# Kernel optimization log

Measured on AMD Instinct MI355X. Metric: run time of the kernel, lower is better.

## Reference

```python
import jax, jax.numpy as jnp
import numpy as np

# Model constants (from init_kwargs, post tensor-parallel split with world_size=8)
N_LOCAL_HEADS = 4      # 32 // 8
N_LOCAL_KV_HEADS = 1   # 8 // 8
N_REP = 4              # local q heads per kv head
HEAD_DIM = 128         # 4096 // 32
ROPE_THETA = 500000.0
EPS = 1e-6
FLOOR_SCALE = 8192.0
ATTN_SCALE = 0.1


def setup_inputs() -> dict:
    key = jax.random.key(0)
    ks = jax.random.split(key, 5)
    B, S, D = 4, 2048, 4096
    x = jax.random.normal(ks[0], (B, S, D), dtype=jnp.float32)
    positions = jnp.arange(S, dtype=jnp.int32)
    w_std = 0.02
    wq = jax.random.normal(ks[1], (D, N_LOCAL_HEADS * HEAD_DIM), dtype=jnp.float32) * w_std
    wk = jax.random.normal(ks[2], (D, N_LOCAL_KV_HEADS * HEAD_DIM), dtype=jnp.float32) * w_std
    wv = jax.random.normal(ks[3], (D, N_LOCAL_KV_HEADS * HEAD_DIM), dtype=jnp.float32) * w_std
    wo = jax.random.normal(ks[4], (N_LOCAL_HEADS * HEAD_DIM, D), dtype=jnp.float32) * w_std
    return {"x": x, "positions": positions, "wq": wq, "wk": wk, "wv": wv, "wo": wo}


def _apply_rope(t, cos, sin):
    # t: [B, S, h, HEAD_DIM]; interleaved complex pairs as in torch view_as_complex
    B, S, h, hd = t.shape
    tr = t.reshape(B, S, h, hd // 2, 2)
    t0, t1 = tr[..., 0], tr[..., 1]
    c = cos[None, :, None, :]  # [1, S, 1, hd//2]
    s = sin[None, :, None, :]
    o0 = t0 * c - t1 * s
    o1 = t0 * s + t1 * c
    return jnp.stack([o0, o1], axis=-1).reshape(B, S, h, hd)


def _rms_norm(t):
    # QK-norm: L2/RMS norm over head_dim, no learnable weight (Llama4 style)
    return t * jax.lax.rsqrt(jnp.mean(t * t, axis=-1, keepdims=True) + EPS)


def reference(x, positions, wq, wk, wv, wo):
    B, S, D = x.shape
    q = (x @ wq).reshape(B, S, N_LOCAL_HEADS, HEAD_DIM)
    k = (x @ wk).reshape(B, S, N_LOCAL_KV_HEADS, HEAD_DIM)
    v = (x @ wv).reshape(B, S, N_LOCAL_KV_HEADS, HEAD_DIM)

    # RoPE angles
    pos_f = positions.astype(jnp.float32)
    inv_freq = 1.0 / (ROPE_THETA ** (jnp.arange(0, HEAD_DIM, 2, dtype=jnp.float32) / HEAD_DIM))
    ang = pos_f[:, None] * inv_freq[None, :]  # [S, HEAD_DIM//2]
    cos, sin = jnp.cos(ang), jnp.sin(ang)

    q = _apply_rope(q, cos, sin)
    k = _apply_rope(k, cos, sin)

    # QK RMSNorm (applied after rope)
    q = _rms_norm(q)
    k = _rms_norm(k)

    # Temperature-tuned query scaling (per absolute position)
    attn_scales = jnp.log(jnp.floor((pos_f + 1.0) / FLOOR_SCALE) + 1.0) * ATTN_SCALE + 1.0
    q = q * attn_scales[None, :, None, None]

    # GQA: repeat kv heads to match local query heads
    k = jnp.repeat(k, N_REP, axis=2)  # [B, S, H, hd]
    v = jnp.repeat(v, N_REP, axis=2)

    scale = 1.0 / jnp.sqrt(jnp.float32(HEAD_DIM))
    scores = jnp.einsum("bqhd,bkhd->bhqk", q, k) * scale  # [B, H, S, S]
    causal = jnp.tril(jnp.ones((S, S), dtype=bool))
    scores = jnp.where(causal[None, None, :, :], scores, jnp.finfo(scores.dtype).min)
    probs = jax.nn.softmax(scores, axis=-1)
    attn = jnp.einsum("bhqk,bkhd->bqhd", probs, v).reshape(B, S, N_LOCAL_HEADS * HEAD_DIM)
    return attn @ wo
```

## Files before the change

kernel.cpp:

```cpp
#include <hip/hip_runtime.h>

typedef unsigned short u16;
typedef unsigned int u32;
typedef __bf16 bf16x8 __attribute__((ext_vector_type(8)));
typedef float f32x4 __attribute__((ext_vector_type(4)));

#define S_LEN 2048

__device__ __forceinline__ u16 f2b(float f) {
    union { float f; unsigned u; } a; a.f = f;
    unsigned u = a.u;
    unsigned r = u + 0x7fffu + ((u >> 16) & 1u);
    return (u16)(r >> 16);
}

__device__ __forceinline__ u32 pk2(float a, float b) {
    return (u32)f2b(a) | ((u32)f2b(b) << 16);
}

__device__ __forceinline__ void gload16(const void* g, void* l) {
    __builtin_amdgcn_global_load_lds(
        (const __attribute__((address_space(1))) unsigned int*)g,
        (__attribute__((address_space(3))) unsigned int*)l,
        16, 0, 0);
}

__global__ __launch_bounds__(256) void conv_x_kernel(const float* __restrict__ x,
                                                     u16* __restrict__ xb) {
    long i = ((long)blockIdx.x * 256 + threadIdx.x) * 4;
    float4 v = *(const float4*)(x + i);
    ushort4 o;
    o.x = f2b(v.x); o.y = f2b(v.y); o.z = f2b(v.z); o.w = f2b(v.w);
    *(ushort4*)(xb + i) = o;
}

__global__ __launch_bounds__(256) void pack_wqkv_kernel(const float* __restrict__ wq,
                                                        const float* __restrict__ wk,
                                                        const float* __restrict__ wv,
                                                        u16* __restrict__ W) {
    __shared__ float t[32][33];
    const int n0 = blockIdx.x * 32, k0 = blockIdx.y * 32;
    const int tid = threadIdx.x;
    const int cc = tid & 31, rr = tid >> 5;
    #pragma unroll
    for (int i = 0; i < 4; ++i) {
        int k = k0 + rr + i * 8, n = n0 + cc;
        float v;
        if (n < 512)      v = wq[(size_t)k * 512 + n];
        else if (n < 640) v = wk[(size_t)k * 128 + (n - 512)];
        else              v = wv[(size_t)k * 128 + (n - 640)];
        t[rr + i * 8][cc] = v;
    }
    __syncthreads();
    #pragma unroll
    for (int i = 0; i < 4; ++i) {
        int nn = rr + i * 8, kk = cc;
        W[(size_t)(n0 + nn) * 4096 + k0 + kk] = f2b(t[kk][nn]);
    }
}

__global__ __launch_bounds__(256) void pack_wo_kernel(const float* __restrict__ wo,
                                                      u16* __restrict__ W) {
    __shared__ float t[32][33];
    const int n0 = blockIdx.x * 32, k0 = blockIdx.y * 32;
    const int tid = threadIdx.x;
    const int cc = tid & 31, rr = tid >> 5;
    #pragma unroll
    for (int i = 0; i < 4; ++i)
        t[rr + i * 8][cc] = wo[(size_t)(k0 + rr + i * 8) * 4096 + n0 + cc];
    __syncthreads();
    #pragma unroll
    for (int i = 0; i < 4; ++i)
        W[(size_t)(n0 + rr + i * 8) * 512 + k0 + cc] = f2b(t[cc][rr + i * 8]);
}

__global__ __launch_bounds__(256) void gemm_bf16(const u16* __restrict__ A,
                                                 const u16* __restrict__ B,
                                                 float* __restrict__ C0,
                                                 float* __restrict__ C1,
                                                 int M, int N, int K, int kLen) {
    __shared__ __align__(16) u16 sA[128 * 32];
    __shared__ __align__(16) u16 sB[128 * 32];
    const int tid = threadIdx.x;
    const int lane = tid & 63, wid = tid >> 6;
    const int wr = wid >> 1, wc = wid & 1;
    const int l15 = lane & 15, g = lane >> 4;
    const int srow = (lane >> 2), scol = (lane & 3) * 8;

    const u32 lid = blockIdx.x + gridDim.x * (blockIdx.y + gridDim.y * blockIdx.z);
    const u32 xcd = lid & 7, slot = lid >> 3;
    const u32 per = gridDim.x * gridDim.z;
    const u32 bml = slot / per;
    const u32 r   = slot - bml * per;
    const int bn  = r % gridDim.x;
    const int z   = r / gridDim.x;
    const int bm  = xcd * (gridDim.y >> 3) + bml;

    float* C = z ? C1 : C0;
    const int k0 = z * kLen;

    f32x4 acc[4][4] = {};

    for (int kt = k0; kt < k0 + kLen; kt += 32) {
        __syncthreads();
        #pragma unroll
        for (int i = 0; i < 2; ++i) {
            int ch = wid * 2 + i;
            int rw = ch * 16 + srow;
            gload16(&A[(size_t)(bm * 128 + rw) * K + kt + scol], &sA[ch * 512]);
            gload16(&B[(size_t)(bn * 128 + rw) * K + kt + scol], &sB[ch * 512]);
        }
        __syncthreads();
        bf16x8 af[4], bfr[4];
        #pragma unroll
        for (int m = 0; m < 4; ++m)
            af[m] = *(const bf16x8*)&sA[(wr * 64 + m * 16 + l15) * 32 + g * 8];
        #pragma unroll
        for (int n = 0; n < 4; ++n)
            bfr[n] = *(const bf16x8*)&sB[(wc * 64 + n * 16 + l15) * 32 + g * 8];
        #pragma unroll
        for (int m = 0; m < 4; ++m)
            #pragma unroll
            for (int n = 0; n < 4; ++n)
                acc[m][n] = __builtin_amdgcn_mfma_f32_16x16x32_bf16(af[m], bfr[n], acc[m][n], 0, 0, 0);
    }

    #pragma unroll
    for (int m = 0; m < 4; ++m) {
        int row = bm * 128 + wr * 64 + m * 16 + g * 4;
        #pragma unroll
        for (int n = 0; n < 4; ++n) {
            int col = bn * 128 + wc * 64 + n * 16 + l15;
            #pragma unroll
            for (int rr = 0; rr < 4; ++rr)
                C[(size_t)(row + rr) * N + col] = acc[m][n][rr];
        }
    }
}

__global__ __launch_bounds__(256) void rope_rms_kernel(const float* __restrict__ P0,
                                                       const float* __restrict__ P1,
                                                       const int* __restrict__ positions,
                                                       u16* __restrict__ Qb,
                                                       u16* __restrict__ Kb) {
    const int w = blockIdx.x * 4 + (threadIdx.x >> 6);
    const int lane = threadIdx.x & 63;
    const int row = w / 5, head = w - row * 5;
    const int s = row & (S_LEN - 1);

    float pos = (float)positions[s];
    float ex = (float)(2 * lane) * (1.0f / 128.0f);
    float inv_freq = __expf(-ex * 13.122363377404328f);
    float ang = pos * inv_freq;
    float c, sn;
    __sincosf(ang, &sn, &c);

    size_t off = (size_t)row * 768 + head * 128 + 2 * lane;
    float2 va = *(const float2*)&P0[off];
    float2 vb = *(const float2*)&P1[off];
    float x0 = va.x + vb.x, x1 = va.y + vb.y;
    float o0 = x0 * c - x1 * sn;
    float o1 = x0 * sn + x1 * c;

    float ss = o0 * o0 + o1 * o1;
    #pragma unroll
    for (int m = 1; m < 64; m <<= 1) ss += __shfl_xor(ss, m, 64);
    float rms = rsqrtf(ss * (1.0f / 128.0f) + 1e-6f);

    if (head < 4) {
        float ascale = logf(floorf((pos + 1.0f) * (1.0f / 8192.0f)) + 1.0f) * 0.1f + 1.0f;
        float mult = rms * ascale * 0.12751743f;
        *(u32*)&Qb[(size_t)row * 512 + head * 128 + 2 * lane] = pk2(o0 * mult, o1 * mult);
    } else {
        *(u32*)&Kb[(size_t)row * 128 + 2 * lane] = pk2(o0 * rms, o1 * rms);
    }
}

__global__ __launch_bounds__(256) void vtrans_kernel(const float* __restrict__ P0,
                                                     const float* __restrict__ P1,
                                                     u16* __restrict__ Vt) {
    __shared__ u16 tile[128][72];
    const int bi = blockIdx.x >> 5, st = blockIdx.x & 31;
    const int s0 = st * 64;
    const int tid = threadIdx.x;
    #pragma unroll
    for (int i = 0; i < 8; ++i) {
        int idx = i * 256 + tid;
        int r = idx >> 5, c4 = idx & 31;
        size_t off = (size_t)(bi * S_LEN + s0 + r) * 768 + 640 + c4 * 4;
        float4 a = *(const float4*)&P0[off];
        float4 b = *(const float4*)&P1[off];
        tile[c4 * 4 + 0][r] = f2b(a.x + b.x);
        tile[c4 * 4 + 1][r] = f2b(a.y + b.y);
        tile[c4 * 4 + 2][r] = f2b(a.z + b.z);
        tile[c4 * 4 + 3][r] = f2b(a.w + b.w);
    }
    __syncthreads();
    #pragma unroll
    for (int i = 0; i < 4; ++i) {
        int idx = i * 256 + tid;
        int d = idx >> 3, sl = idx & 7;
        bf16x8 v = *(const bf16x8*)&tile[d][sl * 8];
        *(bf16x8*)&Vt[((size_t)bi * 128 + d) * S_LEN + s0 + sl * 8] = v;
    }
}

__global__ __launch_bounds__(256) void attn_kernel(const u16* __restrict__ Qb,
                                                   const u16* __restrict__ Kb,
                                                   const u16* __restrict__ Vt,
                                                   u16* __restrict__ Ob) {
    __shared__ __align__(16) u16 sK[2][64 * 128];
    __shared__ __align__(16) u16 sV[2][128 * 64];
    __shared__ __align__(16) u32 p_all[4][16 * 36];
    const int tid = threadIdx.x;
    const int lane = tid & 63, wid = tid >> 6;
    const int l15 = lane & 15, g = lane >> 4;
    const int bid = blockIdx.x;
    const int qt = 127 - (bid >> 2);
    const int b = bid & 3;
    const int h = wid;
    const int q0 = qt * 16;
    const int kswz = (l15 & 7) << 4;

    u32* p_sh = p_all[wid];

    bf16x8 qf[4];
    {
        const u16* qrow = Qb + (size_t)(b * S_LEN + q0 + l15) * 512 + h * 128 + g * 8;
        #pragma unroll
        for (int c = 0; c < 4; ++c) qf[c] = *(const bf16x8*)(qrow + c * 32);
    }
    const u16* Kbase = Kb + (size_t)b * S_LEN * 128;
    const u16* Vbase = Vt + (size_t)b * 128 * S_LEN;

    const int klr = lane >> 4, klo = (lane & 15) * 16;
    const int vlr = lane >> 3, vlo = (lane & 7) * 16;

    auto stage = [&](int buf, int kv0) {
        #pragma unroll
        for (int j = 0; j < 4; ++j) {
            int r0 = wid * 16 + j * 4;
            int row = r0 + klr;
            gload16((const char*)Kbase + (size_t)(kv0 + row) * 256 + (klo ^ ((row & 7) << 4)),
                    &sK[buf][r0 * 128]);
        }
        #pragma unroll
        for (int j = 0; j < 4; ++j) {
            int r0 = wid * 32 + j * 8;
            int row = r0 + vlr;
            gload16((const char*)Vbase + (size_t)row * (S_LEN * 2) + (size_t)kv0 * 2 + (vlo ^ ((row & 7) << 4)),
                    &sV[buf][r0 * 64]);
        }
    };

    f32x4 oacc[8] = {};
    float m_r = -1e30f, l_r = 0.f;

    const int nt = (q0 >> 6) + 1;
    stage(0, 0);
    __syncthreads();

    for (int t = 0; t < nt; ++t) {
        const u16* sKc = sK[t & 1];
        const u16* sVc = sV[t & 1];
        if (t + 1 < nt) stage((t + 1) & 1, (t + 1) * 64);
        const int kv0 = t * 64;
        const bool masked = (t == nt - 1);

        f32x4 sf[4] = {};
        #pragma unroll
        for (int st = 0; st < 4; ++st) {
            #pragma unroll
            for (int c = 0; c < 4; ++c) {
                bf16x8 kf = *(const bf16x8*)((const char*)sKc +
                                (st * 16 + l15) * 256 + ((c * 64 + g * 16) ^ kswz));
                sf[st] = __builtin_amdgcn_mfma_f32_16x16x32_bf16(kf, qf[c], sf[st], 0, 0, 0);
            }
        }
        float p[16];
        #pragma unroll
        for (int st = 0; st < 4; ++st)
            #pragma unroll
            for (int r = 0; r < 4; ++r) p[st * 4 + r] = sf[st][r];
        if (masked) {
            #pragma unroll
            for (int st = 0; st < 4; ++st)
                #pragma unroll
                for (int r = 0; r < 4; ++r) {
                    int kp = kv0 + st * 16 + g * 4 + r;
                    if (kp > q0 + l15) p[st * 4 + r] = -1e30f;
                }
        }
        float tm = p[0];
        #pragma unroll
        for (int i = 1; i < 16; ++i) tm = fmaxf(tm, p[i]);
        tm = fmaxf(tm, __shfl_xor(tm, 16));
        tm = fmaxf(tm, __shfl_xor(tm, 32));
        float mn = fmaxf(m_r, tm);
        float fscale = exp2f(m_r - mn);
        m_r = mn;
        float rs = 0.f;
        #pragma unroll
        for (int i = 0; i < 16; ++i) { p[i] = exp2f(p[i] - mn); rs += p[i]; }
        rs += __shfl_xor(rs, 16);
        rs += __shfl_xor(rs, 32);
        l_r = l_r * fscale + rs;
        #pragma unroll
        for (int ht = 0; ht < 8; ++ht) oacc[ht] *= fscale;

        #pragma unroll
        for (int st = 0; st < 4; ++st) {
            uint2 w;
            w.x = pk2(p[st * 4 + 0], p[st * 4 + 1]);
            w.y = pk2(p[st * 4 + 2], p[st * 4 + 3]);
            *(uint2*)&p_sh[l15 * 36 + st * 8 + g * 2] = w;
        }
        bf16x8 pa0 = *(const bf16x8*)&p_sh[l15 * 36 + g * 4];
        bf16x8 pa1 = *(const bf16x8*)&p_sh[l15 * 36 + 16 + g * 4];

        #pragma unroll
        for (int ht = 0; ht < 8; ++ht) {
            bf16x8 v0 = *(const bf16x8*)((const char*)sVc +
                            (ht * 16 + l15) * 128 + ((g * 16) ^ kswz));
            bf16x8 v1 = *(const bf16x8*)((const char*)sVc +
                            (ht * 16 + l15) * 128 + ((64 + g * 16) ^ kswz));
            oacc[ht] = __builtin_amdgcn_mfma_f32_16x16x32_bf16(v0, pa0, oacc[ht], 0, 0, 0);
            oacc[ht] = __builtin_amdgcn_mfma_f32_16x16x32_bf16(v1, pa1, oacc[ht], 0, 0, 0);
        }
        __syncthreads();
    }

    float inv_l = 1.0f / l_r;
    #pragma unroll
    for (int ht = 0; ht < 8; ++ht) {
        uint2 o;
        o.x = pk2(oacc[ht][0] * inv_l, oacc[ht][1] * inv_l);
        o.y = pk2(oacc[ht][2] * inv_l, oacc[ht][3] * inv_l);
        *(uint2*)&Ob[(size_t)(b * S_LEN + q0 + l15) * 512 + h * 128 + ht * 16 + g * 4] = o;
    }
}

extern "C" void kernel_launch(void* const* d_in, const int* in_sizes, int n_in,
                              void* d_out, int out_size, void* d_ws, size_t ws_size,
                              hipStream_t stream) {
    const float* x         = (const float*)d_in[0];
    const int*   positions = (const int*)d_in[1];
    const float* wq        = (const float*)d_in[2];
    const float* wk        = (const float*)d_in[3];
    const float* wv        = (const float*)d_in[4];
    const float* wo        = (const float*)d_in[5];
    float* out = (float*)d_out;

    u16*   Xb = (u16*)d_out;
    float* P1 = (float*)((char*)d_out + 67108864);

    char* ws = (char*)d_ws;
    size_t off = 0;
    auto alloc = [&](size_t bytes) { void* p = ws + off; off = (off + bytes + 255) & ~(size_t)255; return p; };
    u16*   Wqkv = (u16*)alloc(768ull * 4096 * 2);
    u16*   WoT  = (u16*)alloc(4096ull * 512 * 2);
    float* P0   = (float*)alloc(8192ull * 768 * 4);
    u16*   Qb   = (u16*)alloc(8192ull * 512 * 2);
    u16*   Kb   = (u16*)alloc(8192ull * 128 * 2);
    u16*   Vt   = (u16*)alloc(4ull * 128 * 2048 * 2);
    u16*   Ob   = (u16*)alloc(8192ull * 512 * 2);

    conv_x_kernel<<<(8192 * 4096) / (4 * 256), 256, 0, stream>>>(x, Xb);
    pack_wqkv_kernel<<<dim3(24, 128), 256, 0, stream>>>(wq, wk, wv, Wqkv);
    pack_wo_kernel<<<dim3(128, 16), 256, 0, stream>>>(wo, WoT);

    gemm_bf16<<<dim3(6, 64, 2), 256, 0, stream>>>(Xb, Wqkv, P0, P1, 8192, 768, 4096, 2048);

    rope_rms_kernel<<<(8192 * 5) / 4, 256, 0, stream>>>(P0, P1, positions, Qb, Kb);
    vtrans_kernel<<<128, 256, 0, stream>>>(P0, P1, Vt);

    attn_kernel<<<512, 256, 0, stream>>>(Qb, Kb, Vt, Ob);

    gemm_bf16<<<dim3(32, 64, 1), 256, 0, stream>>>(Ob, WoT, out, nullptr, 8192, 4096, 512, 512);
}
```

Baseline: 270.3 us.

## Fuse fp32-to-bf16 conversion of x into QKV GEMM and double-buffer LDS

Removes the standalone conversion kernel that cast x to bf16 through global memory. The QKV GEMM now loads fp32 x directly into registers, converts it to bf16 and writes it to LDS. Both GEMMs also gain a two-stage LDS double buffer, so the next tile's loads overlap the current tile's MFMAs with one barrier per iteration. The cost is that the QKV GEMM reads twice the A bytes (fp32 instead of bf16) on every tile and holds more registers and LDS.

```diff
diff --git a/kernel.cpp b/kernel.cpp
--- a/kernel.cpp
+++ b/kernel.cpp
@@ -3,6 +3,7 @@
 typedef unsigned short u16;
 typedef unsigned int u32;
 typedef __bf16 bf16x8 __attribute__((ext_vector_type(8)));
+typedef __bf16 bf16x2 __attribute__((ext_vector_type(2)));
 typedef float f32x4 __attribute__((ext_vector_type(4)));
 
 #define S_LEN 2048
@@ -18,20 +19,17 @@
     return (u32)f2b(a) | ((u32)f2b(b) << 16);
 }
 
+__device__ __forceinline__ u32 cvt2(float lo, float hi) {
+    union { bf16x2 v; u32 u; } c;
+    c.v[0] = (__bf16)lo; c.v[1] = (__bf16)hi;
+    return c.u;
+}
+
 __device__ __forceinline__ void gload16(const void* g, void* l) {
     __builtin_amdgcn_global_load_lds(
         (const __attribute__((address_space(1))) unsigned int*)g,
         (__attribute__((address_space(3))) unsigned int*)l,
         16, 0, 0);
-}
-
-__global__ __launch_bounds__(256) void conv_x_kernel(const float* __restrict__ x,
-                                                     u16* __restrict__ xb) {
-    long i = ((long)blockIdx.x * 256 + threadIdx.x) * 4;
-    float4 v = *(const float4*)(x + i);
-    ushort4 o;
-    o.x = f2b(v.x); o.y = f2b(v.y); o.z = f2b(v.z); o.w = f2b(v.w);
-    *(ushort4*)(xb + i) = o;
 }
 
 __global__ __launch_bounds__(256) void pack_wqkv_kernel(const float* __restrict__ wq,
@@ -74,55 +72,98 @@
         W[(size_t)(n0 + rr + i * 8) * 512 + k0 + cc] = f2b(t[cc][rr + i * 8]);
 }
 
-__global__ __launch_bounds__(256) void gemm_bf16(const u16* __restrict__ A,
+template<int CVT>
+__global__ __launch_bounds__(256) void gemm_bf16(const void* __restrict__ Av,
                                                  const u16* __restrict__ B,
                                                  float* __restrict__ C0,
                                                  float* __restrict__ C1,
-                                                 int M, int N, int K, int kLen) {
-    __shared__ __align__(16) u16 sA[128 * 32];
-    __shared__ __align__(16) u16 sB[128 * 32];
+                                                 int N, int K, int kLen) {
+    __shared__ __align__(16) u16 sA[2][128 * 32];
+    __shared__ __align__(16) u16 sB[2][128 * 32];
     const int tid = threadIdx.x;
     const int lane = tid & 63, wid = tid >> 6;
     const int wr = wid >> 1, wc = wid & 1;
     const int l15 = lane & 15, g = lane >> 4;
-    const int srow = (lane >> 2), scol = (lane & 3) * 8;
+    const int srow = lane >> 2, scol = (lane & 3) * 8;
 
     const u32 lid = blockIdx.x + gridDim.x * (blockIdx.y + gridDim.y * blockIdx.z);
     const u32 xcd = lid & 7, slot = lid >> 3;
     const u32 per = gridDim.x * gridDim.z;
     const u32 bml = slot / per;
-    const u32 r   = slot - bml * per;
-    const int bn  = r % gridDim.x;
-    const int z   = r / gridDim.x;
-    const int bm  = xcd * (gridDim.y >> 3) + bml;
+    const u32 rmd = slot - bml * per;
+    const int bn = rmd % gridDim.x;
+    const int z  = rmd / gridDim.x;
+    const int bm = xcd * (gridDim.y >> 3) + bml;
 
     float* C = z ? C1 : C0;
     const int k0 = z * kLen;
+    const int nt = kLen / 32;
+
+    const float* Af = (const float*)Av;
+    const u16*   Ab = (const u16*)Av;
+
+    const int ch0 = wid * 2, ch1 = wid * 2 + 1;
+    const int r0 = ch0 * 16 + srow, r1 = ch1 * 16 + srow;
+
+    auto stageB = [&](int buf, int kt) {
+        gload16(&B[(size_t)(bn * 128 + r0) * K + kt + scol], &sB[buf][ch0 * 512]);
+        gload16(&B[(size_t)(bn * 128 + r1) * K + kt + scol], &sB[buf][ch1 * 512]);
+    };
+    auto stageA_g = [&](int buf, int kt) {
+        gload16(&Ab[(size_t)(bm * 128 + r0) * K + kt + scol], &sA[buf][ch0 * 512]);
+        gload16(&Ab[(size_t)(bm * 128 + r1) * K + kt + scol], &sA[buf][ch1 * 512]);
+    };
+    auto loadA_f = [&](int kt, float4* v) {
+        const float* p0 = &Af[(size_t)(bm * 128 + r0) * K + kt + scol];
+        const float* p1 = &Af[(size_t)(bm * 128 + r1) * K + kt + scol];
+        v[0] = *(const float4*)p0; v[1] = *(const float4*)(p0 + 4);
+        v[2] = *(const float4*)p1; v[3] = *(const float4*)(p1 + 4);
+    };
+    auto writeA_f = [&](int buf, const float4* v) {
+        u32 w0[4] = { cvt2(v[0].x, v[0].y), cvt2(v[0].z, v[0].w),
+                      cvt2(v[1].x, v[1].y), cvt2(v[1].z, v[1].w) };
+        u32 w1[4] = { cvt2(v[2].x, v[2].y), cvt2(v[2].z, v[2].w),
+                      cvt2(v[3].x, v[3].y), cvt2(v[3].z, v[3].w) };
+        *(uint4*)&sA[buf][ch0 * 512 + lane * 8] = *(const uint4*)w0;
+        *(uint4*)&sA[buf][ch1 * 512 + lane * 8] = *(const uint4*)w1;
+    };
 
     f32x4 acc[4][4] = {};
 
-    for (int kt = k0; kt < k0 + kLen; kt += 32) {
-        __syncthreads();
-        #pragma unroll
-        for (int i = 0; i < 2; ++i) {
-            int ch = wid * 2 + i;
-            int rw = ch * 16 + srow;
-            gload16(&A[(size_t)(bm * 128 + rw) * K + kt + scol], &sA[ch * 512]);
-            gload16(&B[(size_t)(bn * 128 + rw) * K + kt + scol], &sB[ch * 512]);
-        }
-        __syncthreads();
+    if (CVT) {
+        float4 v[4];
+        loadA_f(k0, v);
+        writeA_f(0, v);
+    } else {
+        stageA_g(0, k0);
+    }
+    stageB(0, k0);
+    __syncthreads();
+
+    for (int t = 0; t < nt; ++t) {
+        const int cur = t & 1, nxt = cur ^ 1;
+        const int kt = k0 + t * 32;
+        const bool pf = (t + 1 < nt);
+        float4 av[4];
+        if (pf) {
+            if (CVT) loadA_f(kt + 32, av);
+            else     stageA_g(nxt, kt + 32);
+            stageB(nxt, kt + 32);
+        }
         bf16x8 af[4], bfr[4];
         #pragma unroll
         for (int m = 0; m < 4; ++m)
-            af[m] = *(const bf16x8*)&sA[(wr * 64 + m * 16 + l15) * 32 + g * 8];
+            af[m] = *(const bf16x8*)&sA[cur][(wr * 64 + m * 16 + l15) * 32 + g * 8];
         #pragma unroll
         for (int n = 0; n < 4; ++n)
-            bfr[n] = *(const bf16x8*)&sB[(wc * 64 + n * 16 + l15) * 32 + g * 8];
+            bfr[n] = *(const bf16x8*)&sB[cur][(wc * 64 + n * 16 + l15) * 32 + g * 8];
         #pragma unroll
         for (int m = 0; m < 4; ++m)
             #pragma unroll
             for (int n = 0; n < 4; ++n)
                 acc[m][n] = __builtin_amdgcn_mfma_f32_16x16x32_bf16(af[m], bfr[n], acc[m][n], 0, 0, 0);
+        if (pf && CVT) writeA_f(nxt, av);
+        __syncthreads();
     }
 
     #pragma unroll
@@ -351,7 +392,6 @@
     const float* wo        = (const float*)d_in[5];
     float* out = (float*)d_out;
 
-    u16*   Xb = (u16*)d_out;
     float* P1 = (float*)((char*)d_out + 67108864);
 
     char* ws = (char*)d_ws;
@@ -365,16 +405,15 @@
     u16*   Vt   = (u16*)alloc(4ull * 128 * 2048 * 2);
     u16*   Ob   = (u16*)alloc(8192ull * 512 * 2);
 
-    conv_x_kernel<<<(8192 * 4096) / (4 * 256), 256, 0, stream>>>(x, Xb);
     pack_wqkv_kernel<<<dim3(24, 128), 256, 0, stream>>>(wq, wk, wv, Wqkv);
     pack_wo_kernel<<<dim3(128, 16), 256, 0, stream>>>(wo, WoT);
 
-    gemm_bf16<<<dim3(6, 64, 2), 256, 0, stream>>>(Xb, Wqkv, P0, P1, 8192, 768, 4096, 2048);
+    gemm_bf16<1><<<dim3(6, 64, 2), 256, 0, stream>>>(x, Wqkv, P0, P1, 768, 4096, 2048);
 
     rope_rms_kernel<<<(8192 * 5) / 4, 256, 0, stream>>>(P0, P1, positions, Qb, Kb);
     vtrans_kernel<<<128, 256, 0, stream>>>(P0, P1, Vt);
 
     attn_kernel<<<512, 256, 0, stream>>>(Qb, Kb, Vt, Ob);
 
-    gemm_bf16<<<dim3(32, 64, 1), 256, 0, stream>>>(Ob, WoT, out, nullptr, 8192, 4096, 512, 512);
-}
+    gemm_bf16<0><<<dim3(32, 64, 1), 256, 0, stream>>>(Ob, WoT, out, nullptr, 4096, 512, 512);
+}
```

After: 251.6 us. -6.9%, faster.

## Triple-buffer GEMM LDS loads with async prefetch and XOR swizzle

Applied to the files above, without the earlier changes.

Replaces the single-buffered bf16 GEMM with a three-stage LDS ring. Tiles are prefetched two k-steps ahead using global_load_lds, and vmcnt waits replace the double __syncthreads per iteration, so the memory loads overlap with the MFMA work. The LDS column index is also XOR-swizzled on both write and read to cut bank conflicts. The cost is three times the LDS footprint per block, and the code depends on exact vmcnt counting being correct.

```diff
diff --git a/kernel.cpp b/kernel.cpp
--- a/kernel.cpp
+++ b/kernel.cpp
@@ -74,50 +74,63 @@
         W[(size_t)(n0 + rr + i * 8) * 512 + k0 + cc] = f2b(t[cc][rr + i * 8]);
 }
 
-__global__ __launch_bounds__(256) void gemm_bf16(const u16* __restrict__ A,
+__global__ __launch_bounds__(256) void gemm_pipe(const u16* __restrict__ A,
                                                  const u16* __restrict__ B,
                                                  float* __restrict__ C0,
                                                  float* __restrict__ C1,
-                                                 int M, int N, int K, int kLen) {
-    __shared__ __align__(16) u16 sA[128 * 32];
-    __shared__ __align__(16) u16 sB[128 * 32];
+                                                 int N, int K, int kBase) {
+    __shared__ __align__(16) u16 sA[3][128 * 32];
+    __shared__ __align__(16) u16 sB[3][128 * 32];
     const int tid = threadIdx.x;
     const int lane = tid & 63, wid = tid >> 6;
     const int wr = wid >> 1, wc = wid & 1;
     const int l15 = lane & 15, g = lane >> 4;
-    const int srow = (lane >> 2), scol = (lane & 3) * 8;
+    const int srow = lane >> 2;
+    const int swzc = ((lane & 3) * 8) ^ (((lane >> 3) & 3) << 3);
+    const int rswz = ((l15 >> 1) & 3) << 3;
 
     const u32 lid = blockIdx.x + gridDim.x * (blockIdx.y + gridDim.y * blockIdx.z);
     const u32 xcd = lid & 7, slot = lid >> 3;
     const u32 per = gridDim.x * gridDim.z;
     const u32 bml = slot / per;
-    const u32 r   = slot - bml * per;
-    const int bn  = r % gridDim.x;
-    const int z   = r / gridDim.x;
-    const int bm  = xcd * (gridDim.y >> 3) + bml;
+    const u32 rmd = slot - bml * per;
+    const int bn = rmd % gridDim.x;
+    const int z  = rmd / gridDim.x;
+    const int bm = xcd * (gridDim.y >> 3) + bml;
 
     float* C = z ? C1 : C0;
-    const int k0 = z * kLen;
+    const int k0 = z * kBase;
+    const int nt = kBase / 32;
+
+    const int ch0 = wid * 2, ch1 = wid * 2 + 1;
+    const int r0 = ch0 * 16 + srow, r1 = ch1 * 16 + srow;
+
+    auto stage = [&](int buf, int kt) {
+        gload16(&A[(size_t)(bm * 128 + r0) * K + kt + swzc], &sA[buf][ch0 * 512]);
+        gload16(&A[(size_t)(bm * 128 + r1) * K + kt + swzc], &sA[buf][ch1 * 512]);
+        gload16(&B[(size_t)(bn * 128 + r0) * K + kt + swzc], &sB[buf][ch0 * 512]);
+        gload16(&B[(size_t)(bn * 128 + r1) * K + kt + swzc], &sB[buf][ch1 * 512]);
+    };
 
     f32x4 acc[4][4] = {};
 
-    for (int kt = k0; kt < k0 + kLen; kt += 32) {
-        __syncthreads();
-        #pragma unroll
-        for (int i = 0; i < 2; ++i) {
-            int ch = wid * 2 + i;
-            int rw = ch * 16 + srow;
-            gload16(&A[(size_t)(bm * 128 + rw) * K + kt + scol], &sA[ch * 512]);
-            gload16(&B[(size_t)(bn * 128 + rw) * K + kt + scol], &sB[ch * 512]);
-        }
-        __syncthreads();
+    stage(0, k0);
+    stage(1, k0 + 32);
+
+    for (int t = 0; t < nt; ++t) {
+        if (t + 1 < nt) asm volatile("s_waitcnt vmcnt(4)" ::: "memory");
+        else            asm volatile("s_waitcnt vmcnt(0)" ::: "memory");
+        __builtin_amdgcn_s_barrier();
+        __builtin_amdgcn_sched_barrier(0);
+        if (t + 2 < nt) stage((t + 2) % 3, k0 + (t + 2) * 32);
+        const int cur = t % 3;
         bf16x8 af[4], bfr[4];
         #pragma unroll
         for (int m = 0; m < 4; ++m)
-            af[m] = *(const bf16x8*)&sA[(wr * 64 + m * 16 + l15) * 32 + g * 8];
+            af[m] = *(const bf16x8*)&sA[cur][(wr * 64 + m * 16 + l15) * 32 + (g * 8 ^ rswz)];
         #pragma unroll
         for (int n = 0; n < 4; ++n)
-            bfr[n] = *(const bf16x8*)&sB[(wc * 64 + n * 16 + l15) * 32 + g * 8];
+            bfr[n] = *(const bf16x8*)&sB[cur][(wc * 64 + n * 16 + l15) * 32 + (g * 8 ^ rswz)];
         #pragma unroll
         for (int m = 0; m < 4; ++m)
             #pragma unroll
@@ -369,12 +382,12 @@
     pack_wqkv_kernel<<<dim3(24, 128), 256, 0, stream>>>(wq, wk, wv, Wqkv);
     pack_wo_kernel<<<dim3(128, 16), 256, 0, stream>>>(wo, WoT);
 
-    gemm_bf16<<<dim3(6, 64, 2), 256, 0, stream>>>(Xb, Wqkv, P0, P1, 8192, 768, 4096, 2048);
+    gemm_pipe<<<dim3(6, 64, 2), 256, 0, stream>>>(Xb, Wqkv, P0, P1, 768, 4096, 2048);
 
     rope_rms_kernel<<<(8192 * 5) / 4, 256, 0, stream>>>(P0, P1, positions, Qb, Kb);
     vtrans_kernel<<<128, 256, 0, stream>>>(P0, P1, Vt);
 
     attn_kernel<<<512, 256, 0, stream>>>(Qb, Kb, Vt, Ob);
 
-    gemm_bf16<<<dim3(32, 64, 1), 256, 0, stream>>>(Ob, WoT, out, nullptr, 8192, 4096, 512, 512);
-}
+    gemm_pipe<<<dim3(32, 64, 1), 256, 0, stream>>>(Ob, WoT, out, nullptr, 4096, 512, 512);
+}
```

Result: faster. 244.2 us (median of 2 runs) (-9.6%).
